# Kernel optimization log

Measured on AMD Instinct MI355X. Metric: run time of the kernel, lower is better.

## Reference

```python
import jax, jax.numpy as jnp
import numpy as np

# Dims: B samples, D=2048 backbone feature dim (resnet50 fc.in_features),
B, D, G, R, K, C = 16384, 2048, 8, 6, 3, 16


def setup_inputs() -> dict:
    key = jax.random.key(0)
    k0, k1, k2, k3 = jax.random.split(key, 4)
    feats = jax.random.normal(k0, (B, D), dtype=jnp.float32)          # backbone output (dropout=eval identity)
    roi_ids = jax.random.randint(k1, (B,), 0, G)                       # per-sample routing id (roi_names)
    W_reg = jax.random.normal(k2, (G, R, D), dtype=jnp.float32) * 0.02  # reg_heads[roi].weight
    b_reg = jnp.zeros((G, R), dtype=jnp.float32)                       # reg_heads[roi].bias
    W_cls = jax.random.normal(k3, (G, K, C, D), dtype=jnp.float32) * 0.02  # cls_heads[roi][k].weight
    b_cls = jnp.zeros((G, K, C), dtype=jnp.float32)                    # cls_heads[roi][k].bias
    return {"feats": feats, "roi_ids": roi_ids, "W_reg": W_reg, "b_reg": b_reg,
            "W_cls": W_cls, "b_cls": b_cls}


def reference(feats, roi_ids, W_reg, b_reg, W_cls, b_cls):
    # Original loop applies, per sample i, the Linear heads of roi_names[i].
    # Vectorized: compute all-ROI head outputs densely, then gather the routed one.
    # (Same math per sample; dropout is identity in eval mode.)
    reg_all = jnp.einsum('bd,grd->bgr', feats, W_reg) + b_reg[None]        # [B, G, R]
    cls_all = jnp.einsum('bd,gkcd->bgkc', feats, W_cls) + b_cls[None]      # [B, G, K, C]
    reg = jnp.take_along_axis(reg_all, roi_ids[:, None, None], axis=1)[:, 0]            # [B, R]
    cls = jnp.take_along_axis(cls_all, roi_ids[:, None, None, None], axis=1)[:, 0]      # [B, K, C]
    return reg, cls
```

## Files before the change

### kernel.cpp

```cpp
#include <hip/hip_runtime.h>
#include <hip/hip_bf16.h>

#define NB   16384
#define ND   2048
#define NG   8
#define NR   6
#define NKC  48
#define NOUT 54
#define KC2  64
#define NCH2 (ND / KC2)
#define NT16 (NB / 16 + NG)
#define LROW 136
#define BM   32
#define KC   128
#define NCH  (ND / KC)
#define MAXT (NB / BM + NG)

typedef __attribute__((ext_vector_type(8))) short short8_t;
typedef __attribute__((ext_vector_type(4))) float f32x4;

__device__ __forceinline__ unsigned short f2bf(float x) {
    union { float f; unsigned u; } v; v.f = x;
    unsigned r = v.u + 0x7FFFu + ((v.u >> 16) & 1u);
    return (unsigned short)(r >> 16);
}

__device__ __forceinline__ short8_t cvt8(float4 a, float4 b) {
    short8_t s;
    s[0] = (short)f2bf(a.x); s[1] = (short)f2bf(a.y);
    s[2] = (short)f2bf(a.z); s[3] = (short)f2bf(a.w);
    s[4] = (short)f2bf(b.x); s[5] = (short)f2bf(b.y);
    s[6] = (short)f2bf(b.z); s[7] = (short)f2bf(b.w);
    return s;
}

__global__ void hist_kernel(const int* __restrict__ roi, int* __restrict__ counts) {
    int i = blockIdx.x * 256 + threadIdx.x;
    int g = roi[i];
    int lane = threadIdx.x & 63;
    #pragma unroll
    for (int gg = 0; gg < NG; ++gg) {
        unsigned long long m = __ballot(g == gg);
        if (m && lane == (int)(__ffsll((unsigned long long)m) - 1))
            atomicAdd(&counts[gg], (int)__popcll(m));
    }
}

__global__ void scatter_kernel(const int* __restrict__ roi, const int* __restrict__ counts,
                               int* __restrict__ ranks, int* __restrict__ perm) {
    int off[NG];
    int acc = 0;
    #pragma unroll
    for (int gg = 0; gg < NG; ++gg) { off[gg] = acc; acc += counts[gg]; }
    int i = blockIdx.x * 256 + threadIdx.x;
    int g = roi[i];
    int lane = threadIdx.x & 63;
    #pragma unroll
    for (int gg = 0; gg < NG; ++gg) {
        unsigned long long m = __ballot(g == gg);
        if (!m) continue;
        int leader = (int)(__ffsll((unsigned long long)m) - 1);
        int base = 0;
        if (lane == leader) base = atomicAdd(&ranks[gg], (int)__popcll(m));
        base = __shfl(base, leader);
        if (g == gg) {
            int rank = (int)__popcll(m & ((1ull << lane) - 1ull));
            perm[off[gg] + base + rank] = i;
        }
    }
}

__global__ void scatter1_kernel(const int* __restrict__ roi, int* __restrict__ cnt,
                                int* __restrict__ perm) {
    int i = blockIdx.x * 256 + threadIdx.x;
    int g = roi[i];
    int lane = threadIdx.x & 63;
    #pragma unroll
    for (int gg = 0; gg < NG; ++gg) {
        unsigned long long m = __ballot(g == gg);
        if (!m) continue;
        int leader = (int)(__ffsll((unsigned long long)m) - 1);
        int base = 0;
        if (lane == leader) base = atomicAdd(&cnt[gg], (int)__popcll(m));
        base = __shfl(base, leader);
        if (g == gg) {
            int rank = (int)__popcll(m & ((1ull << lane) - 1ull));
            perm[gg * NB + base + rank] = i;
        }
    }
}

__global__ void wconv_kernel(const float* __restrict__ Wreg, const float* __restrict__ Wcls,
                             short* __restrict__ Wbf) {
    int u = blockIdx.x * 256 + threadIdx.x;
    int l = u & 63;
    int q = (u >> 6) & 7;
    int c = (u >> 9) & 31;
    int g = u >> 14;
    int n = q >> 1, ks = q & 1;
    int row = n * 16 + (l & 15);
    int k   = c * 64 + ks * 32 + (l >> 4) * 8;
    short8_t v = {0, 0, 0, 0, 0, 0, 0, 0};
    if (row < NOUT) {
        const float* s = (row < NR) ? Wreg + (size_t)(g * NR + row) * ND + k
                                    : Wcls + (size_t)(g * NKC + row - NR) * ND + k;
        float4 a = *(const float4*)s;
        float4 b = *(const float4*)(s + 4);
        v = cvt8(a, b);
    }
    *(short8_t*)(Wbf + (size_t)u * 8) = v;
}

__launch_bounds__(256, 2)
__global__ void gemm16_kernel(const float* __restrict__ feats,
                              const short* __restrict__ Wbf,
                              const float* __restrict__ breg, const float* __restrict__ bcls,
                              const int* __restrict__ counts, const int* __restrict__ perm,
                              float* __restrict__ out, int stride) {
    int tid = threadIdx.x, w = tid >> 6, l = tid & 63, lr = l & 15, lq = l >> 4;
    int t = blockIdx.x * 4 + w;

    int ts[NG + 1]; ts[0] = 0;
    int off[NG]; int acc_ = 0;
    #pragma unroll
    for (int gg = 0; gg < NG; ++gg) {
        int c = counts[gg];
        off[gg] = stride ? gg * stride : acc_;
        acc_ += c;
        ts[gg + 1] = ts[gg] + (c + 15) / 16;
    }
    if (t >= ts[NG]) return;
    int g = 0;
    #pragma unroll
    for (int gg = 0; gg < NG; ++gg) if (t >= ts[gg + 1]) g = gg + 1;
    int gcnt  = counts[g];
    int goff  = off[g];
    int rbase = (t - ts[g]) * 16;
    int nvalid = gcnt - rbase; if (nvalid > 16) nvalid = 16;

    int r = rbase + lr; if (r >= gcnt) r = gcnt - 1;
    int smp = perm[goff + r];
    const float* aRow  = feats + (size_t)smp * ND;
    const short* bBase = Wbf + (size_t)g * 131072 + l * 8;

    f32x4 ac0 = {0,0,0,0}, ac1 = {0,0,0,0}, ac2 = {0,0,0,0}, ac3 = {0,0,0,0};
    float4   xa0, xa1, xa2, xa3, ya0, ya1, ya2, ya3;
    short8_t xb0, xb1, xb2, xb3, xb4, xb5, xb6, xb7;
    short8_t yb0, yb1, yb2, yb3, yb4, yb5, yb6, yb7;

#define LDA(p, cc) { const float* ap_ = aRow + (cc) * KC2 + lq * 8;            \
        p##0 = *(const float4*)(ap_);      p##1 = *(const float4*)(ap_ + 4);   \
        p##2 = *(const float4*)(ap_ + 32); p##3 = *(const float4*)(ap_ + 36); }
#define LDB(p, cc) { const short* bp_ = bBase + (size_t)(cc) * 4096;           \
        p##0 = *(const short8_t*)(bp_);        p##1 = *(const short8_t*)(bp_ + 512);  \
        p##2 = *(const short8_t*)(bp_ + 1024); p##3 = *(const short8_t*)(bp_ + 1536); \
        p##4 = *(const short8_t*)(bp_ + 2048); p##5 = *(const short8_t*)(bp_ + 2560); \
        p##6 = *(const short8_t*)(bp_ + 3072); p##7 = *(const short8_t*)(bp_ + 3584); }
#define CMP(a, b) { short8_t af0 = cvt8(a##0, a##1), af1 = cvt8(a##2, a##3);   \
        ac0 = __builtin_amdgcn_mfma_f32_16x16x32_bf16(af0, b##0, ac0, 0, 0, 0); \
        ac1 = __builtin_amdgcn_mfma_f32_16x16x32_bf16(af0, b##2, ac1, 0, 0, 0); \
        ac2 = __builtin_amdgcn_mfma_f32_16x16x32_bf16(af0, b##4, ac2, 0, 0, 0); \
        ac3 = __builtin_amdgcn_mfma_f32_16x16x32_bf16(af0, b##6, ac3, 0, 0, 0); \
        ac0 = __builtin_amdgcn_mfma_f32_16x16x32_bf16(af1, b##1, ac0, 0, 0, 0); \
        ac1 = __builtin_amdgcn_mfma_f32_16x16x32_bf16(af1, b##3, ac1, 0, 0, 0); \
        ac2 = __builtin_amdgcn_mfma_f32_16x16x32_bf16(af1, b##5, ac2, 0, 0, 0); \
        ac3 = __builtin_amdgcn_mfma_f32_16x16x32_bf16(af1, b##7, ac3, 0, 0, 0); }

    LDA(xa, 0); LDB(xb, 0);
    #pragma unroll
    for (int c = 0; c < NCH2; c += 2) {
        LDA(ya, c + 1); LDB(yb, c + 1);
        CMP(xa, xb);
        if (c + 2 < NCH2) { LDA(xa, c + 2); LDB(xb, c + 2); }
        CMP(ya, yb);
    }
#undef LDA
#undef LDB
#undef CMP

    const int B6 = NB * NR;
    #pragma unroll
    for (int n = 0; n < 4; ++n) {
        f32x4 v = (n == 0) ? ac0 : (n == 1) ? ac1 : (n == 2) ? ac2 : ac3;
        int col = n * 16 + lr;
        if (col < NOUT) {
            #pragma unroll
            for (int j = 0; j < 4; ++j) {
                int row = lq * 4 + j;
                if (row < nvalid) {
                    int s2 = perm[goff + rbase + row];
                    if (col < NR) out[s2 * NR + col] = v[j] + breg[g * NR + col];
                    else          out[B6 + s2 * NKC + (col - NR)] = v[j] + bcls[g * NKC + (col - NR)];
                }
            }
        }
    }
}

__launch_bounds__(256, 3)
__global__ void gemm_kernel(const float* __restrict__ feats,
                            const float* __restrict__ Wreg, const float* __restrict__ breg,
                            const float* __restrict__ Wcls, const float* __restrict__ bcls,
                            const int* __restrict__ counts, const int* __restrict__ perm,
                            float* __restrict__ out, int stride) {
    __shared__ __align__(16) short Bsh[2][64][LROW];
    __shared__ int sRow[BM];

    int ts[NG + 1]; ts[0] = 0;
    int off[NG]; int acc = 0;
    #pragma unroll
    for (int gg = 0; gg < NG; ++gg) {
        int c = counts[gg];
        off[gg] = stride ? gg * stride : acc;
        acc += c;
        ts[gg + 1] = ts[gg] + (c + BM - 1) / BM;
    }
    int b = blockIdx.x;
    if (b >= ts[NG]) return;
    int g = 0;
    #pragma unroll
    for (int gg = 0; gg < NG; ++gg) if (b >= ts[gg + 1]) g = gg + 1;
    int gcnt  = counts[g];
    int goff  = off[g];
    int rbase = (b - ts[g]) * BM;
    int nvalid = gcnt - rbase; if (nvalid > BM) nvalid = BM;

    int tid = threadIdx.x;
    if (tid < BM) {
        int r = rbase + tid;
        if (r >= gcnt) r = gcnt - 1;
        sRow[tid] = perm[goff + r];
    }
    __syncthreads();

    int rB = tid >> 2;
    int cq = tid & 3;
    const float* wsrc = nullptr;
    if (rB < NR)        wsrc = Wreg + ((size_t)g * NR + rB) * ND + cq * 32;
    else if (rB < NOUT) wsrc = Wcls + ((size_t)g * NKC + (rB - NR)) * ND + cq * 32;

    int w = tid >> 6, l = tid & 63, lr = l & 15, lq = l >> 4;
    int mt = w & 1, nh = w >> 1;
    const float* aptr = feats + (size_t)sRow[mt * 16 + lr] * ND + lq * 8;
    const short* brp = (const short*)&Bsh[0][0][0] + (nh * 32 + lr) * LROW + lq * 8;

    f32x4 acc0 = {0, 0, 0, 0}, acc1 = {0, 0, 0, 0};
    float4 rb[8];

    if (wsrc) {
        #pragma unroll
        for (int i = 0; i < 8; ++i) rb[i] = *(const float4*)(wsrc + 4 * i);
    } else {
        #pragma unroll
        for (int i = 0; i < 8; ++i) rb[i] = make_float4(0.f, 0.f, 0.f, 0.f);
    }
    {
        short* bw = &Bsh[0][rB][cq * 32];
        #pragma unroll
        for (int j = 0; j < 4; ++j) *(short8_t*)(bw + 8 * j) = cvt8(rb[2 * j], rb[2 * j + 1]);
    }
    __syncthreads();

    #pragma unroll
    for (int c = 0; c < NCH; ++c) {
        const int cur = c & 1, nxt = cur ^ 1;
        if (c + 1 < NCH && wsrc) {
            const float* s = wsrc + (c + 1) * KC;
            #pragma unroll
            for (int i = 0; i < 8; ++i) rb[i] = *(const float4*)(s + 4 * i);
        }
        const short* bp = brp + cur * (64 * LROW);
        const float* ap = aptr + c * KC;
        #pragma unroll
        for (int ks = 0; ks < 4; ++ks) {
            float4 a0 = *(const float4*)(ap + ks * 32);
            float4 a1 = *(const float4*)(ap + ks * 32 + 4);
            short8_t af = cvt8(a0, a1);
            short8_t b0 = *(const short8_t*)(bp + ks * 32);
            short8_t b1 = *(const short8_t*)(bp + 16 * LROW + ks * 32);
            acc0 = __builtin_amdgcn_mfma_f32_16x16x32_bf16(af, b0, acc0, 0, 0, 0);
            acc1 = __builtin_amdgcn_mfma_f32_16x16x32_bf16(af, b1, acc1, 0, 0, 0);
        }
        if (c + 1 < NCH && wsrc) {
            short* bw = &Bsh[nxt][rB][cq * 32];
            #pragma unroll
            for (int j = 0; j < 4; ++j) *(short8_t*)(bw + 8 * j) = cvt8(rb[2 * j], rb[2 * j + 1]);
        } else if (c + 1 < NCH) {
            short8_t z = {0,0,0,0,0,0,0,0};
            short* bw = &Bsh[nxt][rB][cq * 32];
            #pragma unroll
            for (int j = 0; j < 4; ++j) *(short8_t*)(bw + 8 * j) = z;
        }
        __syncthreads();
    }

    const int B6 = NB * NR;
    #pragma unroll
    for (int n = 0; n < 2; ++n) {
        f32x4 v = n ? acc1 : acc0;
        int col = nh * 32 + n * 16 + lr;
        if (col < NOUT) {
            #pragma unroll
            for (int j = 0; j < 4; ++j) {
                int row = mt * 16 + lq * 4 + j;
                if (row < nvalid) {
                    int smp = sRow[row];
                    if (col < NR) out[smp * NR + col] = v[j] + breg[g * NR + col];
                    else          out[B6 + smp * NKC + (col - NR)] = v[j] + bcls[g * NKC + (col - NR)];
                }
            }
        }
    }
}

__global__ void fallback_kernel(const float* __restrict__ feats, const int* __restrict__ roi,
                                const float* __restrict__ Wreg, const float* __restrict__ breg,
                                const float* __restrict__ Wcls, const float* __restrict__ bcls,
                                float* __restrict__ out) {
    int i = blockIdx.x;
    int lane = threadIdx.x;
    int g = roi[i];
    const float* frow = feats + (size_t)i * ND;
    float f[32];
    #pragma unroll
    for (int q = 0; q < 32; ++q) f[q] = frow[lane + 64 * q];
    for (int o = 0; o < NOUT; ++o) {
        const float* wrow = (o < NR) ? Wreg + ((size_t)g * NR + o) * ND
                                     : Wcls + ((size_t)g * NKC + (o - NR)) * ND;
        float p = 0.f;
        #pragma unroll
        for (int q = 0; q < 32; ++q) p += f[q] * wrow[lane + 64 * q];
        #pragma unroll
        for (int s = 32; s; s >>= 1) p += __shfl_xor(p, s);
        if (lane == 0) {
            if (o < NR) out[i * NR + o] = p + breg[g * NR + o];
            else        out[NB * NR + i * NKC + (o - NR)] = p + bcls[g * NKC + (o - NR)];
        }
    }
}

extern "C" void kernel_launch(void* const* d_in, const int* in_sizes, int n_in,
                              void* d_out, int out_size, void* d_ws, size_t ws_size,
                              hipStream_t stream) {
    const float* feats = (const float*)d_in[0];
    const int*   roi   = (const int*)d_in[1];
    const float* Wreg  = (const float*)d_in[2];
    const float* breg  = (const float*)d_in[3];
    const float* Wcls  = (const float*)d_in[4];
    const float* bcls  = (const float*)d_in[5];
    float* out = (float*)d_out;

    const size_t wbfBytes = (size_t)NG * 131072 * 2;
    const size_t need_t1 = wbfBytes + 256 + (size_t)NG * NB * 4;
    const size_t need_t3 = 256 + (size_t)NB * 4;

    if (ws_size >= need_t1) {
        short* Wbf = (short*)d_ws;
        int* cnt  = (int*)((char*)d_ws + wbfBytes);
        int* perm = cnt + 64;
        hipMemsetAsync(cnt, 0, 8 * sizeof(int), stream);
        wconv_kernel<<<512, 256, 0, stream>>>(Wreg, Wcls, Wbf);
        scatter1_kernel<<<NB / 256, 256, 0, stream>>>(roi, cnt, perm);
        gemm16_kernel<<<(NT16 + 3) / 4, 256, 0, stream>>>(feats, Wbf, breg, bcls, cnt, perm, out, NB);
    } else if (ws_size >= need_t3) {
        int* counts = (int*)d_ws;
        int* ranks  = counts + 8;
        int* perm   = counts + 64;
        hipMemsetAsync(counts, 0, 16 * sizeof(int), stream);
        hist_kernel<<<NB / 256, 256, 0, stream>>>(roi, counts);
        scatter_kernel<<<NB / 256, 256, 0, stream>>>(roi, counts, ranks, perm);
        gemm_kernel<<<MAXT, 256, 0, stream>>>(feats, Wreg, breg, Wcls, bcls, counts, perm, out, 0);
    } else {
        fallback_kernel<<<NB, 64, 0, stream>>>(feats, roi, Wreg, breg, Wcls, bcls, out);
    }
}
```

Before: 83.93 us.

## Stage GEMM operands through LDS with async global_load_lds triple buffering

```diff
diff --git a/kernel.cpp b/kernel.cpp
--- a/kernel.cpp
+++ b/kernel.cpp
@@ -33,6 +33,16 @@
     s[6] = (short)f2bf(b.z); s[7] = (short)f2bf(b.w);
     return s;
 }
+
+__device__ __forceinline__ void gl_lds16(const void* g, void* s) {
+    __builtin_amdgcn_global_load_lds(
+        (const __attribute__((address_space(1))) void*)g,
+        (__attribute__((address_space(3))) void*)s,
+        16, 0, 0);
+}
+
+#define WAITV(N) do { asm volatile("s_waitcnt vmcnt(" #N ")" ::: "memory"); \
+                      __builtin_amdgcn_sched_barrier(0); } while (0)
 
 __global__ void hist_kernel(const int* __restrict__ roi, int* __restrict__ counts) {
     int i = blockIdx.x * 256 + threadIdx.x;
@@ -111,14 +121,17 @@
     *(short8_t*)(Wbf + (size_t)u * 8) = v;
 }
 
-__launch_bounds__(256, 2)
-__global__ void gemm16_kernel(const float* __restrict__ feats,
-                              const short* __restrict__ Wbf,
-                              const float* __restrict__ breg, const float* __restrict__ bcls,
-                              const int* __restrict__ counts, const int* __restrict__ perm,
-                              float* __restrict__ out, int stride) {
-    int tid = threadIdx.x, w = tid >> 6, l = tid & 63, lr = l & 15, lq = l >> 4;
-    int t = blockIdx.x * 4 + w;
+__launch_bounds__(64, 1)
+__global__ void gemm_pipe_kernel(const float* __restrict__ feats,
+                                 const short* __restrict__ Wbf,
+                                 const float* __restrict__ breg, const float* __restrict__ bcls,
+                                 const int* __restrict__ counts, const int* __restrict__ perm,
+                                 float* __restrict__ out, int stride) {
+    __shared__ __align__(16) char lds[3][12288];
+
+    int l = threadIdx.x;
+    int lr = l & 15, lq = l >> 4;
+    int t = blockIdx.x;
 
     int ts[NG + 1]; ts[0] = 0;
     int off[NG]; int acc_ = 0;
@@ -140,48 +153,55 @@
 
     int r = rbase + lr; if (r >= gcnt) r = gcnt - 1;
     int smp = perm[goff + r];
-    const float* aRow  = feats + (size_t)smp * ND;
+    const float* aRow  = feats + (size_t)smp * ND + lq * 8;
     const short* bBase = Wbf + (size_t)g * 131072 + l * 8;
 
-    f32x4 ac0 = {0,0,0,0}, ac1 = {0,0,0,0}, ac2 = {0,0,0,0}, ac3 = {0,0,0,0};
-    float4   xa0, xa1, xa2, xa3, ya0, ya1, ya2, ya3;
-    short8_t xb0, xb1, xb2, xb3, xb4, xb5, xb6, xb7;
-    short8_t yb0, yb1, yb2, yb3, yb4, yb5, yb6, yb7;
-
-#define LDA(p, cc) { const float* ap_ = aRow + (cc) * KC2 + lq * 8;            \
-        p##0 = *(const float4*)(ap_);      p##1 = *(const float4*)(ap_ + 4);   \
-        p##2 = *(const float4*)(ap_ + 32); p##3 = *(const float4*)(ap_ + 36); }
-#define LDB(p, cc) { const short* bp_ = bBase + (size_t)(cc) * 4096;           \
-        p##0 = *(const short8_t*)(bp_);        p##1 = *(const short8_t*)(bp_ + 512);  \
-        p##2 = *(const short8_t*)(bp_ + 1024); p##3 = *(const short8_t*)(bp_ + 1536); \
-        p##4 = *(const short8_t*)(bp_ + 2048); p##5 = *(const short8_t*)(bp_ + 2560); \
-        p##6 = *(const short8_t*)(bp_ + 3072); p##7 = *(const short8_t*)(bp_ + 3584); }
-#define CMP(a, b) { short8_t af0 = cvt8(a##0, a##1), af1 = cvt8(a##2, a##3);   \
-        ac0 = __builtin_amdgcn_mfma_f32_16x16x32_bf16(af0, b##0, ac0, 0, 0, 0); \
-        ac1 = __builtin_amdgcn_mfma_f32_16x16x32_bf16(af0, b##2, ac1, 0, 0, 0); \
-        ac2 = __builtin_amdgcn_mfma_f32_16x16x32_bf16(af0, b##4, ac2, 0, 0, 0); \
-        ac3 = __builtin_amdgcn_mfma_f32_16x16x32_bf16(af0, b##6, ac3, 0, 0, 0); \
-        ac0 = __builtin_amdgcn_mfma_f32_16x16x32_bf16(af1, b##1, ac0, 0, 0, 0); \
-        ac1 = __builtin_amdgcn_mfma_f32_16x16x32_bf16(af1, b##3, ac1, 0, 0, 0); \
-        ac2 = __builtin_amdgcn_mfma_f32_16x16x32_bf16(af1, b##5, ac2, 0, 0, 0); \
-        ac3 = __builtin_amdgcn_mfma_f32_16x16x32_bf16(af1, b##7, ac3, 0, 0, 0); }
-
-    LDA(xa, 0); LDB(xb, 0);
-    #pragma unroll
-    for (int c = 0; c < NCH2; c += 2) {
-        LDA(ya, c + 1); LDB(yb, c + 1);
-        CMP(xa, xb);
-        if (c + 2 < NCH2) { LDA(xa, c + 2); LDB(xb, c + 2); }
-        CMP(ya, yb);
-    }
-#undef LDA
-#undef LDB
-#undef CMP
+    f32x4 acc[4] = {{0,0,0,0},{0,0,0,0},{0,0,0,0},{0,0,0,0}};
+
+#define STAGE(cc, sl) do {                                                    \
+        const float* a_ = aRow + (cc) * KC2;                                  \
+        gl_lds16(a_,      &lds[sl][0]);                                       \
+        gl_lds16(a_ + 4,  &lds[sl][1024]);                                    \
+        gl_lds16(a_ + 32, &lds[sl][2048]);                                    \
+        gl_lds16(a_ + 36, &lds[sl][3072]);                                    \
+        const short* b_ = bBase + (size_t)(cc) * 4096;                        \
+        gl_lds16(b_,        &lds[sl][4096]);                                  \
+        gl_lds16(b_ +  512, &lds[sl][5120]);                                  \
+        gl_lds16(b_ + 1024, &lds[sl][6144]);                                  \
+        gl_lds16(b_ + 1536, &lds[sl][7168]);                                  \
+        gl_lds16(b_ + 2048, &lds[sl][8192]);                                  \
+        gl_lds16(b_ + 2560, &lds[sl][9216]);                                  \
+        gl_lds16(b_ + 3072, &lds[sl][10240]);                                 \
+        gl_lds16(b_ + 3584, &lds[sl][11264]);                                 \
+    } while (0)
+
+    STAGE(0, 0); STAGE(1, 1); STAGE(2, 2);
+
+    #pragma unroll
+    for (int c = 0; c < NCH2; ++c) {
+        const int sl = c % 3;
+        if (c <= NCH2 - 3)      { WAITV(24); }
+        else if (c == NCH2 - 2) { WAITV(12); }
+        else                    { WAITV(0);  }
+        #pragma unroll
+        for (int ks = 0; ks < 2; ++ks) {
+            float4 a0 = *(const float4*)&lds[sl][ks * 2048 + l * 16];
+            float4 a1 = *(const float4*)&lds[sl][ks * 2048 + 1024 + l * 16];
+            short8_t af = cvt8(a0, a1);
+            #pragma unroll
+            for (int n = 0; n < 4; ++n) {
+                short8_t bf = *(const short8_t*)&lds[sl][4096 + (n * 2 + ks) * 1024 + l * 16];
+                acc[n] = __builtin_amdgcn_mfma_f32_16x16x32_bf16(af, bf, acc[n], 0, 0, 0);
+            }
+        }
+        if (c + 3 < NCH2) STAGE(c + 3, sl);
+    }
+#undef STAGE
 
     const int B6 = NB * NR;
     #pragma unroll
     for (int n = 0; n < 4; ++n) {
-        f32x4 v = (n == 0) ? ac0 : (n == 1) ? ac1 : (n == 2) ? ac2 : ac3;
+        f32x4 v = acc[n];
         int col = n * 16 + lr;
         if (col < NOUT) {
             #pragma unroll
@@ -361,7 +381,7 @@
         hipMemsetAsync(cnt, 0, 8 * sizeof(int), stream);
         wconv_kernel<<<512, 256, 0, stream>>>(Wreg, Wcls, Wbf);
         scatter1_kernel<<<NB / 256, 256, 0, stream>>>(roi, cnt, perm);
-        gemm16_kernel<<<(NT16 + 3) / 4, 256, 0, stream>>>(feats, Wbf, breg, bcls, cnt, perm, out, NB);
+        gemm_pipe_kernel<<<NT16, 64, 0, stream>>>(feats, Wbf, breg, bcls, cnt, perm, out, NB);
     } else if (ws_size >= need_t3) {
         int* counts = (int*)d_ws;
         int* ranks  = counts + 8;
```

Result: slower. 91.47 us (+9.0%).

## Split K across four waves per 16-row tile with shared-memory reduction

Applied to the files above, without the earlier changes.

```diff
diff --git a/kernel.cpp b/kernel.cpp
--- a/kernel.cpp
+++ b/kernel.cpp
@@ -7,8 +7,9 @@
 #define NR   6
 #define NKC  48
 #define NOUT 54
+#define KW   512
 #define KC2  64
-#define NCH2 (ND / KC2)
+#define NCW  (KW / KC2)
 #define NT16 (NB / 16 + NG)
 #define LROW 136
 #define BM   32
@@ -111,14 +112,16 @@
     *(short8_t*)(Wbf + (size_t)u * 8) = v;
 }
 
-__launch_bounds__(256, 2)
-__global__ void gemm16_kernel(const float* __restrict__ feats,
-                              const short* __restrict__ Wbf,
-                              const float* __restrict__ breg, const float* __restrict__ bcls,
-                              const int* __restrict__ counts, const int* __restrict__ perm,
-                              float* __restrict__ out, int stride) {
+__launch_bounds__(256, 4)
+__global__ void gemm_ks_kernel(const float* __restrict__ feats,
+                               const short* __restrict__ Wbf,
+                               const float* __restrict__ breg, const float* __restrict__ bcls,
+                               const int* __restrict__ counts, const int* __restrict__ perm,
+                               float* __restrict__ out, int stride) {
+    __shared__ float sacc[3][16][66];
+
     int tid = threadIdx.x, w = tid >> 6, l = tid & 63, lr = l & 15, lq = l >> 4;
-    int t = blockIdx.x * 4 + w;
+    int t = blockIdx.x;
 
     int ts[NG + 1]; ts[0] = 0;
     int off[NG]; int acc_ = 0;
@@ -140,57 +143,64 @@
 
     int r = rbase + lr; if (r >= gcnt) r = gcnt - 1;
     int smp = perm[goff + r];
-    const float* aRow  = feats + (size_t)smp * ND;
-    const short* bBase = Wbf + (size_t)g * 131072 + l * 8;
-
-    f32x4 ac0 = {0,0,0,0}, ac1 = {0,0,0,0}, ac2 = {0,0,0,0}, ac3 = {0,0,0,0};
-    float4   xa0, xa1, xa2, xa3, ya0, ya1, ya2, ya3;
-    short8_t xb0, xb1, xb2, xb3, xb4, xb5, xb6, xb7;
-    short8_t yb0, yb1, yb2, yb3, yb4, yb5, yb6, yb7;
-
-#define LDA(p, cc) { const float* ap_ = aRow + (cc) * KC2 + lq * 8;            \
-        p##0 = *(const float4*)(ap_);      p##1 = *(const float4*)(ap_ + 4);   \
-        p##2 = *(const float4*)(ap_ + 32); p##3 = *(const float4*)(ap_ + 36); }
-#define LDB(p, cc) { const short* bp_ = bBase + (size_t)(cc) * 4096;           \
-        p##0 = *(const short8_t*)(bp_);        p##1 = *(const short8_t*)(bp_ + 512);  \
-        p##2 = *(const short8_t*)(bp_ + 1024); p##3 = *(const short8_t*)(bp_ + 1536); \
-        p##4 = *(const short8_t*)(bp_ + 2048); p##5 = *(const short8_t*)(bp_ + 2560); \
-        p##6 = *(const short8_t*)(bp_ + 3072); p##7 = *(const short8_t*)(bp_ + 3584); }
-#define CMP(a, b) { short8_t af0 = cvt8(a##0, a##1), af1 = cvt8(a##2, a##3);   \
-        ac0 = __builtin_amdgcn_mfma_f32_16x16x32_bf16(af0, b##0, ac0, 0, 0, 0); \
-        ac1 = __builtin_amdgcn_mfma_f32_16x16x32_bf16(af0, b##2, ac1, 0, 0, 0); \
-        ac2 = __builtin_amdgcn_mfma_f32_16x16x32_bf16(af0, b##4, ac2, 0, 0, 0); \
-        ac3 = __builtin_amdgcn_mfma_f32_16x16x32_bf16(af0, b##6, ac3, 0, 0, 0); \
-        ac0 = __builtin_amdgcn_mfma_f32_16x16x32_bf16(af1, b##1, ac0, 0, 0, 0); \
-        ac1 = __builtin_amdgcn_mfma_f32_16x16x32_bf16(af1, b##3, ac1, 0, 0, 0); \
-        ac2 = __builtin_amdgcn_mfma_f32_16x16x32_bf16(af1, b##5, ac2, 0, 0, 0); \
-        ac3 = __builtin_amdgcn_mfma_f32_16x16x32_bf16(af1, b##7, ac3, 0, 0, 0); }
-
-    LDA(xa, 0); LDB(xb, 0);
-    #pragma unroll
-    for (int c = 0; c < NCH2; c += 2) {
-        LDA(ya, c + 1); LDB(yb, c + 1);
-        CMP(xa, xb);
-        if (c + 2 < NCH2) { LDA(xa, c + 2); LDB(xb, c + 2); }
-        CMP(ya, yb);
-    }
-#undef LDA
-#undef LDB
-#undef CMP
-
-    const int B6 = NB * NR;
-    #pragma unroll
-    for (int n = 0; n < 4; ++n) {
-        f32x4 v = (n == 0) ? ac0 : (n == 1) ? ac1 : (n == 2) ? ac2 : ac3;
-        int col = n * 16 + lr;
-        if (col < NOUT) {
-            #pragma unroll
-            for (int j = 0; j < 4; ++j) {
-                int row = lq * 4 + j;
-                if (row < nvalid) {
-                    int s2 = perm[goff + rbase + row];
-                    if (col < NR) out[s2 * NR + col] = v[j] + breg[g * NR + col];
-                    else          out[B6 + s2 * NKC + (col - NR)] = v[j] + bcls[g * NKC + (col - NR)];
+    const float* aRow  = feats + (size_t)smp * ND + w * KW + lq * 8;
+    const short* bBase = Wbf + (size_t)g * 131072 + (size_t)w * NCW * 4096 + l * 8;
+
+    f32x4 acc[4] = {{0,0,0,0},{0,0,0,0},{0,0,0,0},{0,0,0,0}};
+
+    #pragma unroll
+    for (int c = 0; c < NCW; ++c) {
+        const float* ap = aRow + c * KC2;
+        float4 a0 = *(const float4*)(ap);
+        float4 a1 = *(const float4*)(ap + 4);
+        float4 a2 = *(const float4*)(ap + 32);
+        float4 a3 = *(const float4*)(ap + 36);
+        const short* bp = bBase + (size_t)c * 4096;
+        short8_t b0 = *(const short8_t*)(bp);
+        short8_t b1 = *(const short8_t*)(bp + 512);
+        short8_t b2 = *(const short8_t*)(bp + 1024);
+        short8_t b3 = *(const short8_t*)(bp + 1536);
+        short8_t b4 = *(const short8_t*)(bp + 2048);
+        short8_t b5 = *(const short8_t*)(bp + 2560);
+        short8_t b6 = *(const short8_t*)(bp + 3072);
+        short8_t b7 = *(const short8_t*)(bp + 3584);
+        short8_t af0 = cvt8(a0, a1);
+        short8_t af1 = cvt8(a2, a3);
+        acc[0] = __builtin_amdgcn_mfma_f32_16x16x32_bf16(af0, b0, acc[0], 0, 0, 0);
+        acc[1] = __builtin_amdgcn_mfma_f32_16x16x32_bf16(af0, b2, acc[1], 0, 0, 0);
+        acc[2] = __builtin_amdgcn_mfma_f32_16x16x32_bf16(af0, b4, acc[2], 0, 0, 0);
+        acc[3] = __builtin_amdgcn_mfma_f32_16x16x32_bf16(af0, b6, acc[3], 0, 0, 0);
+        acc[0] = __builtin_amdgcn_mfma_f32_16x16x32_bf16(af1, b1, acc[0], 0, 0, 0);
+        acc[1] = __builtin_amdgcn_mfma_f32_16x16x32_bf16(af1, b3, acc[1], 0, 0, 0);
+        acc[2] = __builtin_amdgcn_mfma_f32_16x16x32_bf16(af1, b5, acc[2], 0, 0, 0);
+        acc[3] = __builtin_amdgcn_mfma_f32_16x16x32_bf16(af1, b7, acc[3], 0, 0, 0);
+    }
+
+    if (w > 0) {
+        #pragma unroll
+        for (int n = 0; n < 4; ++n)
+            #pragma unroll
+            for (int j = 0; j < 4; ++j)
+                sacc[w - 1][lq * 4 + j][n * 16 + lr] = acc[n][j];
+    }
+    __syncthreads();
+
+    if (w == 0) {
+        const int B6 = NB * NR;
+        #pragma unroll
+        for (int n = 0; n < 4; ++n) {
+            int col = n * 16 + lr;
+            if (col < NOUT) {
+                #pragma unroll
+                for (int j = 0; j < 4; ++j) {
+                    int row = lq * 4 + j;
+                    if (row < nvalid) {
+                        float v = acc[n][j]
+                                + sacc[0][row][col] + sacc[1][row][col] + sacc[2][row][col];
+                        int s2 = perm[goff + rbase + row];
+                        if (col < NR) out[s2 * NR + col] = v + breg[g * NR + col];
+                        else          out[B6 + s2 * NKC + (col - NR)] = v + bcls[g * NKC + (col - NR)];
+                    }
                 }
             }
         }
@@ -361,7 +371,7 @@
         hipMemsetAsync(cnt, 0, 8 * sizeof(int), stream);
         wconv_kernel<<<512, 256, 0, stream>>>(Wreg, Wcls, Wbf);
         scatter1_kernel<<<NB / 256, 256, 0, stream>>>(roi, cnt, perm);
-        gemm16_kernel<<<(NT16 + 3) / 4, 256, 0, stream>>>(feats, Wbf, breg, bcls, cnt, perm, out, NB);
+        gemm_ks_kernel<<<NT16, 256, 0, stream>>>(feats, Wbf, breg, bcls, cnt, perm, out, NB);
     } else if (ws_size >= need_t3) {
         int* counts = (int*)d_ws;
         int* ranks  = counts + 8;
```

Measured after the change: 73.53 us. -12.4%, faster.
